# Kernel optimization log

Hardware: AMD Instinct MI355X
Metric: run time of the kernel (lower is better)

## Reference

```python
import jax, jax.numpy as jnp
import numpy as np

B, T, C, H = 8, 4096, 384, 64

def setup_inputs() -> dict:
    key = jax.random.key(0)
    k1, k2, k3, k4 = jax.random.split(key, 4)
    x = jax.random.normal(k1, (B, T, C), dtype=jnp.float32)
    # nn.Linear(C, H, bias=False) weight applied as x @ W (W stored [C, H])
    s = 1.0 / np.sqrt(C)
    Wk = jax.random.normal(k2, (C, H), dtype=jnp.float32) * s
    Wq = jax.random.normal(k3, (C, H), dtype=jnp.float32) * s
    Wv = jax.random.normal(k4, (C, H), dtype=jnp.float32) * s
    return {"x": x, "Wk": Wk, "Wq": Wq, "Wv": Wv}

def reference(x, Wk, Wq, Wv):
    Bx, Tx, Cx = x.shape
    k = x @ Wk  # [B,T,H]
    q = x @ Wq  # [B,T,H]
    v = x @ Wv  # [B,T,H]
    # NOTE: original scales by C**-0.5 (embedding dim), not head_size**-0.5
    w = jnp.einsum('bth,bsh->bts', q, k) * (Cx ** -0.5)  # [B,T,T]
    causal = jnp.tril(jnp.ones((Tx, Tx), dtype=bool))
    w = jnp.where(causal, w, -jnp.inf)
    w = jax.nn.softmax(w, axis=-1)
    # dropout omitted (eval mode / deterministic reference)
    out = jnp.einsum('bts,bsh->bth', w, v)  # [B,T,H]
    return out
```

## Files before the change

kernel.cpp:

```cpp
#include <hip/hip_runtime.h>
#include <hip/hip_bf16.h>


typedef __bf16 bf16x8 __attribute__((ext_vector_type(8)));
typedef float  f32x4  __attribute__((ext_vector_type(4)));

#define BB   8
#define TT   4096
#define CC   384
#define HH   64
#define NROW (BB*TT)
#define QSCALE (0.05103103630798288f * 1.4426950408889634f)

#if __has_builtin(__builtin_amdgcn_exp2f)
#define EXP2(x) __builtin_amdgcn_exp2f(x)
#else
#define EXP2(x) exp2f(x)
#endif

__device__ __forceinline__ unsigned short f2bf(float f) {
    __bf16 h = (__bf16)f;
    return __builtin_bit_cast(unsigned short, h);
}

__global__ __launch_bounds__(256) void wtrans_kernel(
        const float* __restrict__ Wk,
        const float* __restrict__ Wq,
        const float* __restrict__ Wv,
        unsigned short* __restrict__ Wt) {
    __shared__ __align__(16) unsigned short tile[64][72];
    const float* Wm = (blockIdx.y == 0) ? Wk : ((blockIdx.y == 1) ? Wq : Wv);
    unsigned short* Wtm = Wt + blockIdx.y * (HH * CC);
    const int c0 = blockIdx.x * 64;
#pragma unroll
    for (int i = 0; i < 16; ++i) {
        int id = threadIdx.x + i * 256;
        int c = id >> 6, h = id & 63;
        tile[c][h] = f2bf(Wm[(c0 + c) * HH + h]);
    }
    __syncthreads();
#pragma unroll
    for (int i = 0; i < 16; ++i) {
        int id = threadIdx.x + i * 256;
        int h = id >> 6, c = id & 63;
        Wtm[h * CC + c0 + c] = tile[c][h];
    }
}

__global__ __launch_bounds__(256, 1) void qkv_kernel(
        const float* __restrict__ x,
        const unsigned short* __restrict__ Wt,
        unsigned short* __restrict__ q_ws,
        unsigned short* __restrict__ k_ws,
        unsigned short* __restrict__ vt_ws) {
    __shared__ __align__(16) float xs2[2][32][64];
    __shared__ __align__(16) unsigned short wts[2][3][64][64];
    __shared__ __align__(16) unsigned short vtile[64][40];

    const int lane = threadIdx.x & 63;
    const int wv   = threadIdx.x >> 6;
    const int rt   = wv & 1;
    const int hh   = wv >> 1;
    const int l15  = lane & 15;
    const int quad = lane >> 4;
    const int rb   = blockIdx.x * 32;
    const int ntb  = hh * 2;

    auto stageX = [&](int kk, int bb) {
#pragma unroll
        for (int j = 0; j < 2; ++j) {
            const int r0 = wv * 8 + j * 4;
            const int r  = r0 + quad;
            const int ch = l15 ^ (r & 7);
            const float* src = x + (long)(rb + r) * CC + kk * 64 + ch * 4;
            float* dst = &xs2[bb][r0][0];
            __builtin_amdgcn_global_load_lds(
                (const __attribute__((address_space(1))) unsigned int*)src,
                (__attribute__((address_space(3))) unsigned int*)dst,
                16, 0, 0);
        }
    };

    auto stageW = [&](int kk, int bb) {
#pragma unroll
        for (int i = 0; i < 6; ++i) {
            const int j   = wv + 4 * i;
            const int m   = j >> 3;
            const int rg  = j & 7;
            const int h   = rg * 8 + (lane >> 3);
            const int chs = (lane & 7) ^ (h & 7);
            const unsigned short* src =
                Wt + m * (HH * CC) + h * CC + kk * 64 + chs * 8;
            unsigned short* dst = &wts[bb][m][rg * 8][0];
            __builtin_amdgcn_global_load_lds(
                (const __attribute__((address_space(1))) unsigned int*)src,
                (__attribute__((address_space(3))) unsigned int*)dst,
                16, 0, 0);
        }
    };

    f32x4 acc[3][2];
    const f32x4 zero = {0.f, 0.f, 0.f, 0.f};
#pragma unroll
    for (int m = 0; m < 3; ++m)
#pragma unroll
        for (int n = 0; n < 2; ++n) acc[m][n] = zero;

    const int rloc = rt * 16 + l15;
    const int rx7  = rloc & 7;
    const int hx7  = l15 & 7;

    stageX(0, 0);
    stageW(0, 0);
    __asm volatile("s_waitcnt vmcnt(0)" ::: "memory");
    __syncthreads();

#pragma unroll
    for (int kk = 0; kk < 6; ++kk) {
        const int cur = kk & 1;
        if (kk < 5) { stageX(kk + 1, cur ^ 1); stageW(kk + 1, cur ^ 1); }
#pragma unroll
        for (int h01 = 0; h01 < 2; ++h01) {
            const int chb = 8 * h01 + 2 * quad;
            const f32x4 xa = *reinterpret_cast<const f32x4*>(
                &xs2[cur][rloc][((chb) ^ rx7) * 4]);
            const f32x4 xb = *reinterpret_cast<const f32x4*>(
                &xs2[cur][rloc][((chb + 1) ^ rx7) * 4]);
            bf16x8 a;
#pragma unroll
            for (int e = 0; e < 4; ++e) {
                a[e]     = (__bf16)xa[e];
                a[4 + e] = (__bf16)xb[e];
            }
#pragma unroll
            for (int m = 0; m < 3; ++m)
#pragma unroll
                for (int n = 0; n < 2; ++n) {
                    const int hN = (ntb + n) * 16 + l15;
                    const bf16x8 bfr = *reinterpret_cast<const bf16x8*>(
                        &wts[cur][m][hN][(((h01 << 2) + quad) ^ hx7) << 3]);
                    acc[m][n] = __builtin_amdgcn_mfma_f32_16x16x32_bf16(
                        a, bfr, acc[m][n], 0, 0, 0);
                }
        }
        __asm volatile("s_waitcnt vmcnt(0)" ::: "memory");
        __syncthreads();
    }

#pragma unroll
    for (int n = 0; n < 2; ++n) {
        const int nt = ntb + n;
        const int h  = nt * 16 + l15;
        const int c8 = h >> 3;
        const int jj = h & 7;
#pragma unroll
        for (int r = 0; r < 4; ++r) {
            const int gr = rb + rt * 16 + quad * 4 + r;
            const int s   = gr & 63;
            const int stp = ((s >> 4) & 2) + ((s >> 2) & 1);
            const int ip  = ((s >> 1) & 12) + (s & 3);
            k_ws[(long)(gr >> 6) * 4096 + stp * 1024 + c8 * 128 + ip * 8 + jj]
                = f2bf(acc[0][n][r]);
            q_ws[gr * HH + h] = f2bf(acc[1][n][r] * QSCALE);
            vtile[h][rt * 16 + quad * 4 + r] = f2bf(acc[2][n][r]);
        }
    }
    __syncthreads();
    {
        const int id  = threadIdx.x;
        const int dt  = id >> 6, scl = (id >> 4) & 3, ii = id & 15;
        const int sc  = scl + ((rb >> 3) & 4);
        unsigned short* dst = vt_ws + (long)(rb >> 6) * 4096
                              + (dt * 8 + sc) * 128 + ii * 8;
        *reinterpret_cast<uint4*>(dst) =
            *reinterpret_cast<const uint4*>(&vtile[dt * 16 + ii][scl * 8]);
    }
}

__global__ __launch_bounds__(1024, 4) void attn_kernel(
        const unsigned short* __restrict__ q_ws,
        const unsigned short* __restrict__ k_ws,
        const unsigned short* __restrict__ vt_ws,
        float* __restrict__ out) {
    __shared__ __align__(16) unsigned short kvbuf[2][4][8192];
    __shared__ __align__(16) float xchg[64 * 65];
    __shared__ float mx1[64], lx1[64];

    const int lane = threadIdx.x & 63;
    const int wv16 = threadIdx.x >> 6;
    const int grp  = wv16 >> 2;
    const int wg   = wv16 & 3;
    const int l15  = lane & 15;
    const int quad = lane >> 4;

    const int bid = blockIdx.x;
    const int b   = bid & 7;
    const int p   = bid >> 3;

    const f32x4 zero = {0.f, 0.f, 0.f, 0.f};

    auto stage_round = [&](int j, int bb, int qt) {
        const int tg = 4 * j + grp;
        if (tg > qt) return;
        const int qq = wg;
        const char* srcb;
        int dstoff;
        if (qq < 2) {
            srcb = (const char*)(k_ws + ((long)((b * TT + tg * 64) >> 4)) * 1024)
                   + qq * 4096;
            dstoff = qq * 4096;
        } else {
            srcb = (const char*)(vt_ws + ((long)((b * TT + tg * 64) >> 6)) * 4096)
                   + (qq - 2) * 4096;
            dstoff = 8192 + (qq - 2) * 4096;
        }
        char* dstb = (char*)&kvbuf[bb][grp][0] + dstoff;
#pragma unroll
        for (int i = 0; i < 4; ++i) {
            __builtin_amdgcn_global_load_lds(
                (const __attribute__((address_space(1))) unsigned int*)
                    (srcb + i * 1024 + lane * 16),
                (__attribute__((address_space(3))) unsigned int*)(dstb + i * 1024),
                16, 0, 0);
        }
    };

    auto do_tile = [&](int t, int qt, int qrow, int cur,
                       const bf16x8& qf0, const bf16x8& qf1,
                       f32x4* o, float& mprev, float& lsum) {
        const int s0 = t * 64;
        const unsigned short* kvt = &kvbuf[cur][grp][0];

        bf16x8 ka0[4], ka1[4];
#pragma unroll
        for (int st = 0; st < 4; ++st) {
            ka0[st] = *reinterpret_cast<const bf16x8*>(
                kvt + st * 1024 + lane * 8);
            ka1[st] = *reinterpret_cast<const bf16x8*>(
                kvt + st * 1024 + 512 + lane * 8);
        }
        bf16x8 vb0[4], vb1[4];
#pragma unroll
        for (int dt = 0; dt < 4; ++dt) {
            vb0[dt] = *reinterpret_cast<const bf16x8*>(
                kvt + 4096 + dt * 1024 + lane * 8);
            vb1[dt] = *reinterpret_cast<const bf16x8*>(
                kvt + 4096 + dt * 1024 + 512 + lane * 8);
        }

        f32x4 sc[4];
        __builtin_amdgcn_s_setprio(1);
#pragma unroll
        for (int st = 0; st < 4; ++st) {
            f32x4 z = zero;
            z = __builtin_amdgcn_mfma_f32_16x16x32_bf16(ka0[st], qf0, z, 0, 0, 0);
            z = __builtin_amdgcn_mfma_f32_16x16x32_bf16(ka1[st], qf1, z, 0, 0, 0);
            sc[st] = z;
        }
        __builtin_amdgcn_s_setprio(0);

        if (t == qt) {
#pragma unroll
            for (int st = 0; st < 4; ++st)
#pragma unroll
                for (int r = 0; r < 4; ++r) {
                    int sg = s0 + ((st >> 1) << 5) + (quad << 3)
                               + ((st & 1) << 2) + r;
                    if (sg > qrow) sc[st][r] = -1e30f;
                }
        }

        float mloc = -1e30f;
#pragma unroll
        for (int st = 0; st < 4; ++st)
#pragma unroll
            for (int r = 0; r < 4; ++r) mloc = fmaxf(mloc, sc[st][r]);
        mloc = fmaxf(mloc, __shfl_xor(mloc, 16));
        mloc = fmaxf(mloc, __shfl_xor(mloc, 32));

        if (!__all(mloc <= mprev + 8.0f)) {
            const float mnew = fmaxf(mprev, mloc);
            const float alpha = EXP2(mprev - mnew);
            lsum *= alpha;
            float ar[4];
#pragma unroll
            for (int r = 0; r < 4; ++r) ar[r] = __shfl(alpha, quad * 4 + r);
#pragma unroll
            for (int dt = 0; dt < 4; ++dt)
#pragma unroll
                for (int r = 0; r < 4; ++r) o[dt][r] *= ar[r];
            mprev = mnew;
        }

        float psum = 0.f;
#pragma unroll
        for (int st = 0; st < 4; ++st)
#pragma unroll
            for (int r = 0; r < 4; ++r) {
                float pv = EXP2(sc[st][r] - mprev);
                psum += pv;
                sc[st][r] = pv;
            }
        lsum += psum;

        bf16x8 pf0, pf1;
#pragma unroll
        for (int r = 0; r < 4; ++r) {
            pf0[r]     = (__bf16)sc[0][r];
            pf0[4 + r] = (__bf16)sc[1][r];
            pf1[r]     = (__bf16)sc[2][r];
            pf1[4 + r] = (__bf16)sc[3][r];
        }
        __builtin_amdgcn_s_setprio(1);
#pragma unroll
        for (int dt = 0; dt < 4; ++dt) {
            o[dt] = __builtin_amdgcn_mfma_f32_16x16x32_bf16(pf0, vb0[dt], o[dt], 0, 0, 0);
            o[dt] = __builtin_amdgcn_mfma_f32_16x16x32_bf16(pf1, vb1[dt], o[dt], 0, 0, 0);
        }
        __builtin_amdgcn_s_setprio(0);
    };

    auto merge_store = [&](int qt, f32x4* o, float& mprev, float& lsum) {
        lsum += __shfl_xor(lsum, 16);
        lsum += __shfl_xor(lsum, 32);
        for (int rr = 1; rr < 4; ++rr) {
            __syncthreads();
            if (grp == rr) {
                if (quad == 0) { mx1[wg * 16 + l15] = mprev; lx1[wg * 16 + l15] = lsum; }
#pragma unroll
                for (int dt = 0; dt < 4; ++dt)
#pragma unroll
                    for (int r = 0; r < 4; ++r)
                        xchg[(wg * 16 + quad * 4 + r) * 65 + dt * 16 + l15] = o[dt][r];
            }
            __syncthreads();
            if (grp == 0) {
#pragma unroll
                for (int r = 0; r < 4; ++r) {
                    const int row = wg * 16 + quad * 4 + r;
                    const float m0r = __shfl(mprev, quad * 4 + r);
                    const float m1r = mx1[row];
                    const float ms  = fmaxf(m0r, m1r);
                    const float w0  = EXP2(m0r - ms);
                    const float w1  = EXP2(m1r - ms);
#pragma unroll
                    for (int dt = 0; dt < 4; ++dt)
                        o[dt][r] = o[dt][r] * w0 + xchg[row * 65 + dt * 16 + l15] * w1;
                }
                const float m1l = mx1[wg * 16 + l15];
                const float msl = fmaxf(mprev, m1l);
                lsum = EXP2(mprev - msl) * lsum + EXP2(m1l - msl) * lx1[wg * 16 + l15];
                mprev = msl;
            }
        }
        if (grp == 0) {
            float rl[4];
#pragma unroll
            for (int r = 0; r < 4; ++r) rl[r] = 1.0f / __shfl(lsum, quad * 4 + r);
            const int orow = qt * 64 + wg * 16 + quad * 4;
#pragma unroll
            for (int dt = 0; dt < 4; ++dt)
#pragma unroll
                for (int r = 0; r < 4; ++r)
                    out[(long)(b * TT + orow + r) * HH + dt * 16 + l15] = o[dt][r] * rl[r];
        }
        __syncthreads();
    };

    auto run_phase = [&](int qt) {
        const int qrow = qt * 64 + wg * 16 + l15;
        const unsigned short* qbase = q_ws + (b * TT + qrow) * HH;
        const bf16x8 qf0 = *reinterpret_cast<const bf16x8*>(qbase + quad * 8);
        const bf16x8 qf1 = *reinterpret_cast<const bf16x8*>(qbase + 32 + quad * 8);
        f32x4 o[4];
#pragma unroll
        for (int dt = 0; dt < 4; ++dt) o[dt] = zero;
        float mprev = -1e30f, lsum = 0.f;

        const int rounds = (qt >> 2) + 1;
        int cur = 0;
        stage_round(0, 0, qt);
        __asm volatile("s_waitcnt vmcnt(0)" ::: "memory");
        __syncthreads();
        for (int j = 0; j < rounds; ++j) {
            if (j + 1 < rounds) stage_round(j + 1, cur ^ 1, qt);
            __asm volatile("" ::: "memory");
            const int t = 4 * j + grp;
            if (t <= qt) do_tile(t, qt, qrow, cur, qf0, qf1, o, mprev, lsum);
            __asm volatile("s_waitcnt vmcnt(0)" ::: "memory");
            __syncthreads();
            cur ^= 1;
        }
        merge_store(qt, o, mprev, lsum);
    };

    run_phase(63 - p);
    run_phase(p);
}

extern "C" void kernel_launch(void* const* d_in, const int* in_sizes, int n_in,
                              void* d_out, int out_size, void* d_ws, size_t ws_size,
                              hipStream_t stream) {
    const float* x  = (const float*)d_in[0];
    const float* Wk = (const float*)d_in[1];
    const float* Wq = (const float*)d_in[2];
    const float* Wv = (const float*)d_in[3];
    float* out = (float*)d_out;

    char* ws = (char*)d_ws;
    unsigned short* Wt    = (unsigned short*)(ws);
    unsigned short* q_ws  = (unsigned short*)(ws + 147456);
    unsigned short* k_ws  = (unsigned short*)(ws + 147456 + 4194304);
    unsigned short* vt_ws = (unsigned short*)(ws + 147456 + 2 * 4194304);

    wtrans_kernel<<<dim3(6, 3), 256, 0, stream>>>(Wk, Wq, Wv, Wt);
    qkv_kernel<<<NROW / 32, 256, 0, stream>>>(x, Wt, q_ws, k_ws, vt_ws);
    attn_kernel<<<(TT / 128) * BB, 1024, 0, stream>>>(q_ws, k_ws, vt_ws, out);
}
```

Measured before the change: 141.2 us.

## Drop K/V double buffering and alias LDS to allow two blocks per CU

Replaces the double-buffered K/V LDS staging with a single 64KB buffer, and overlays the merge scratch arrays (xchg, mx1, lx1) onto that same region. Staging for each round now happens synchronously before compute, with a barrier around it. The aim is to cut LDS per block enough that two 1024-thread blocks fit on a CU, relying on the second block to hide load latency. In exchange, the in-block overlap of loads with compute is lost. It also risks a race where the merge scratch overwrites K/V data while another wave group is still reading it, unless the merge step synchronizes first.

```diff
diff --git a/kernel.cpp b/kernel.cpp
--- a/kernel.cpp
+++ b/kernel.cpp
@@ -182,9 +182,11 @@
         const unsigned short* __restrict__ k_ws,
         const unsigned short* __restrict__ vt_ws,
         float* __restrict__ out) {
-    __shared__ __align__(16) unsigned short kvbuf[2][4][8192];
-    __shared__ __align__(16) float xchg[64 * 65];
-    __shared__ float mx1[64], lx1[64];
+    __shared__ __align__(16) char smem[65536];
+    unsigned short* kvbase = (unsigned short*)smem;
+    float* xchg = (float*)smem;
+    float* mx1  = (float*)(smem + 16640);
+    float* lx1  = (float*)(smem + 16896);
 
     const int lane = threadIdx.x & 63;
     const int wv16 = threadIdx.x >> 6;
@@ -199,22 +201,21 @@
 
     const f32x4 zero = {0.f, 0.f, 0.f, 0.f};
 
-    auto stage_round = [&](int j, int bb, int qt) {
+    auto stage_round = [&](int j, int qt) {
         const int tg = 4 * j + grp;
         if (tg > qt) return;
-        const int qq = wg;
         const char* srcb;
         int dstoff;
-        if (qq < 2) {
+        if (wg < 2) {
             srcb = (const char*)(k_ws + ((long)((b * TT + tg * 64) >> 4)) * 1024)
-                   + qq * 4096;
-            dstoff = qq * 4096;
+                   + wg * 4096;
+            dstoff = wg * 4096;
         } else {
             srcb = (const char*)(vt_ws + ((long)((b * TT + tg * 64) >> 6)) * 4096)
-                   + (qq - 2) * 4096;
-            dstoff = 8192 + (qq - 2) * 4096;
-        }
-        char* dstb = (char*)&kvbuf[bb][grp][0] + dstoff;
+                   + (wg - 2) * 4096;
+            dstoff = 8192 + (wg - 2) * 4096;
+        }
+        char* dstb = (char*)kvbase + grp * 16384 + dstoff;
 #pragma unroll
         for (int i = 0; i < 4; ++i) {
             __builtin_amdgcn_global_load_lds(
@@ -225,11 +226,11 @@
         }
     };
 
-    auto do_tile = [&](int t, int qt, int qrow, int cur,
+    auto do_tile = [&](int t, int qt, int qrow,
                        const bf16x8& qf0, const bf16x8& qf1,
                        f32x4* o, float& mprev, float& lsum) {
         const int s0 = t * 64;
-        const unsigned short* kvt = &kvbuf[cur][grp][0];
+        const unsigned short* kvt = kvbase + grp * 8192;
 
         bf16x8 ka0[4], ka1[4];
 #pragma unroll
@@ -378,18 +379,13 @@
         float mprev = -1e30f, lsum = 0.f;
 
         const int rounds = (qt >> 2) + 1;
-        int cur = 0;
-        stage_round(0, 0, qt);
-        __asm volatile("s_waitcnt vmcnt(0)" ::: "memory");
-        __syncthreads();
         for (int j = 0; j < rounds; ++j) {
-            if (j + 1 < rounds) stage_round(j + 1, cur ^ 1, qt);
-            __asm volatile("" ::: "memory");
-            const int t = 4 * j + grp;
-            if (t <= qt) do_tile(t, qt, qrow, cur, qf0, qf1, o, mprev, lsum);
+            if (j > 0) __syncthreads();
+            stage_round(j, qt);
             __asm volatile("s_waitcnt vmcnt(0)" ::: "memory");
             __syncthreads();
-            cur ^= 1;
+            const int t = 4 * j + grp;
+            if (t <= qt) do_tile(t, qt, qrow, qf0, qf1, o, mprev, lsum);
         }
         merge_store(qt, o, mprev, lsum);
     };
```

Result: slower. 147.3 us (+4.3%).
